# Optimization experiments

Measured on AMD Instinct MI355X. Metric: run time of the kernel, lower is better.

Reference implementation:

```python
import jax, jax.numpy as jnp
import numpy as np

N_Q = 8  # number of residual quantization levels


def setup_inputs() -> dict:
    key = jax.random.key(0)
    k1, k2 = jax.random.split(key)
    hidden_states = jax.random.normal(k1, (8192, 128), dtype=jnp.float32)
    codebooks = jax.random.normal(k2, (N_Q, 256, 128), dtype=jnp.float32)
    return {"hidden_states": hidden_states, "codebooks": codebooks}


def reference(hidden_states, codebooks):
    """Residual VQ encode: per level, nearest codebook entry by L2, subtract, accumulate.

    hidden_states: [N, D]; codebooks: [n_q, bins, D].
    Returns (codes [n_q, N] int, quantized [N, D]).
    """
    residual = hidden_states
    quantized = jnp.zeros_like(hidden_states)
    codes = []
    for i in range(N_Q):  # small fixed loop over structurally distinct levels
        codebook = codebooks[i]  # [bins, D]
        # squared L2 distance, same math as the original broadcasted form
        dist = jnp.sum((residual[:, None, :] - codebook[None, :, :]) ** 2, axis=-1)  # [N, bins]
        idx = jnp.argmin(dist, axis=-1)  # [N]
        chosen = codebook[idx]  # [N, D]
        quantized = quantized + chosen
        residual = residual - chosen
        codes.append(idx)
    return jnp.stack(codes, axis=0), quantized
```

## Files before the change

### kernel.cpp

```cpp
#include <hip/hip_runtime.h>

#define NQ 8
#define BINS 256
#define D 128
#define RPB 32
#define THREADS 1024
#define RSTRIDE 132
#define FREG 520

typedef short s8v __attribute__((ext_vector_type(8)));
typedef short s4v __attribute__((ext_vector_type(4)));
typedef float f4v __attribute__((ext_vector_type(4)));

static __device__ __forceinline__ unsigned short bf16_rtne(float x) {
    unsigned u = __float_as_uint(x);
    unsigned r = (u + 0x7fffu + ((u >> 16) & 1u)) >> 16;
    return (unsigned short)r;
}
static __device__ __forceinline__ float bf16_to_f(unsigned short h) {
    return __uint_as_float(((unsigned)h) << 16);
}
struct Split3 { short h, m, l; };
static __device__ __forceinline__ Split3 split3(float x) {
    Split3 s;
    unsigned short hb = bf16_rtne(x);
    float r1 = x - bf16_to_f(hb);
    unsigned short mb = bf16_rtne(r1);
    unsigned short lb = bf16_rtne(r1 - bf16_to_f(mb));
    s.h = (short)hb; s.m = (short)mb; s.l = (short)lb;
    return s;
}
static __device__ __forceinline__ unsigned long long u64min(unsigned long long a, unsigned long long b) {
    return a < b ? a : b;
}
static __device__ __forceinline__ unsigned dpp_row_min16(unsigned v) {
    unsigned t;
    t = (unsigned)__builtin_amdgcn_update_dpp(0, (int)v, 0xB1,  0xF, 0xF, true); v = v < t ? v : t;
    t = (unsigned)__builtin_amdgcn_update_dpp(0, (int)v, 0x4E,  0xF, 0xF, true); v = v < t ? v : t;
    t = (unsigned)__builtin_amdgcn_update_dpp(0, (int)v, 0x124, 0xF, 0xF, true); v = v < t ? v : t;
    t = (unsigned)__builtin_amdgcn_update_dpp(0, (int)v, 0x128, 0xF, 0xF, true); v = v < t ? v : t;
    return v;
}

__global__ __launch_bounds__(256) void rvq_prep(
    const float* __restrict__ cb, short* __restrict__ cb_hi,
    short* __restrict__ cb_mid, short* __restrict__ cb_lo,
    float* __restrict__ c2)
{
    __shared__ float st[16 * RSTRIDE];
    const int L = blockIdx.x >> 4;
    const int o = blockIdx.x & 15;
    const int t = threadIdx.x;

    const float4* src = (const float4*)(cb + ((size_t)L * BINS + o * 16) * D);
    #pragma unroll
    for (int i = 0; i < 2; ++i) {
        int f4 = i * 256 + t;
        int row = f4 >> 5, c4 = f4 & 31;
        float4 v = src[f4];
        float* d = &st[row * RSTRIDE + c4 * 4];
        d[0] = v.x; d[1] = v.y; d[2] = v.z; d[3] = v.w;
    }
    __syncthreads();

    const int bin = t >> 4;
    const int kc  = t & 15;
    const float* p = &st[bin * RSTRIDE + kc * 8];
    s8v h8, m8, l8;
    float s = 0.f;
    #pragma unroll
    for (int j = 0; j < 8; ++j) {
        float x = p[j];
        Split3 sp = split3(x);
        h8[j] = sp.h; m8[j] = sp.m; l8[j] = sp.l;
        s = fmaf(x, x, s);
    }
    int idx = (L * 16 + kc) * BINS + (o * 16 + bin);
    ((s8v*)cb_hi)[idx]  = h8;
    ((s8v*)cb_mid)[idx] = m8;
    ((s8v*)cb_lo)[idx]  = l8;
    s += __shfl_xor(s, 1, 64);
    s += __shfl_xor(s, 2, 64);
    s += __shfl_xor(s, 4, 64);
    s += __shfl_xor(s, 8, 64);
    if (kc == 0) c2[L * BINS + o * 16 + bin] = s;
}

static __device__ __forceinline__ void frag_store4(
    const float* rres, short* ah, short* am, short* al, int rr_, int g8, int half)
{
    s4v h4, m4, l4;
    #pragma unroll
    for (int j = 0; j < 4; ++j) {
        Split3 sp = split3(rres[j]);
        h4[j] = sp.h; m4[j] = sp.m; l4[j] = sp.l;
    }
    int q  = g8 & 3;
    int ks = g8 >> 2;
    int mt = rr_ >> 4;
    int r16 = rr_ & 15;
    int idx16 = q * 16 + ((r16 + 4 * q) & 15);
    int off = (mt * 4 + ks) * FREG + idx16 * 8 + half * 4;
    *(s4v*)&ah[off] = h4;
    *(s4v*)&am[off] = m4;
    *(s4v*)&al[off] = l4;
}

static __device__ __forceinline__ void issue_b(
    int lv, int bin, int quad,
    const s8v* __restrict__ bhp, const s8v* __restrict__ bmp, const s8v* __restrict__ blp,
    const float* __restrict__ c2p,
    s8v bh[4], s8v bm[4], s8v bl[4], float& c2v)
{
    c2v = c2p[lv * BINS + bin];
    #pragma unroll
    for (int ks = 0; ks < 4; ++ks) {
        int idx = (lv * 16 + ks * 4 + quad) * BINS + bin;
        bh[ks] = bhp[idx];
        bm[ks] = bmp[idx];
        bl[ks] = blp[idx];
    }
}

__global__ __launch_bounds__(THREADS, 4) void rvq_kernel(
    const float* __restrict__ hidden,
    const float* __restrict__ cb_f32,
    const short* __restrict__ cb_hi,
    const short* __restrict__ cb_mid,
    const short* __restrict__ cb_lo,
    const float* __restrict__ c2p,
    float* __restrict__ out_codes,
    float* __restrict__ out_quant,
    int N)
{
    __shared__ __align__(16) short ah[8 * FREG];
    __shared__ __align__(16) short am[8 * FREG];
    __shared__ __align__(16) short al[8 * FREG];
    __shared__ __align__(16) unsigned long long redw[RPB][18];

    const int t = threadIdx.x;
    const int w = t >> 6;
    const int l = t & 63;
    const int quad = l >> 4;
    const int m = l & 15;
    const int row0 = blockIdx.x * RPB;
    const int woff = w * 16;
    const int bin = woff + m;
    const int rr_  = t >> 5;
    const int gd   = t & 31;
    const int g8   = gd >> 1;
    const int half = gd & 1;
    const int dbase = g8 * 8 + half * 4;

    float rres[4], hreg[4];
    {
        const float4* hp = (const float4*)(hidden + (size_t)(row0 + rr_) * D + dbase);
        float4 v = *hp;
        hreg[0] = v.x; hreg[1] = v.y; hreg[2] = v.z; hreg[3] = v.w;
        rres[0] = v.x; rres[1] = v.y; rres[2] = v.z; rres[3] = v.w;
    }
    frag_store4(rres, ah, am, al, rr_, g8, half);

    const s8v* bhp = (const s8v*)cb_hi;
    const s8v* bmp = (const s8v*)cb_mid;
    const s8v* blp = (const s8v*)cb_lo;

    s8v bh[4], bm[4], bl[4];
    float c2v;
    issue_b(0, bin, quad, bhp, bmp, blp, c2p, bh, bm, bl, c2v);

    for (int level = 0; level < NQ; ++level) {
        __syncthreads();

        unsigned ucand[2][4];
        const int idx16 = quad * 16 + ((m + 4 * quad) & 15);
        #pragma unroll
        for (int mt = 0; mt < 2; ++mt) {
            f4v a0 = {0.f, 0.f, 0.f, 0.f};
            f4v a1 = {0.f, 0.f, 0.f, 0.f};
            f4v a2 = {0.f, 0.f, 0.f, 0.f};
            #pragma unroll
            for (int ks = 0; ks < 4; ++ks) {
                int off = (mt * 4 + ks) * FREG + idx16 * 8;
                s8v afh = *(const s8v*)&ah[off];
                s8v afm = *(const s8v*)&am[off];
                s8v afl = *(const s8v*)&al[off];
                a0 = __builtin_amdgcn_mfma_f32_16x16x32_bf16(afh, bh[ks], a0, 0, 0, 0);
                a1 = __builtin_amdgcn_mfma_f32_16x16x32_bf16(afh, bm[ks], a1, 0, 0, 0);
                a1 = __builtin_amdgcn_mfma_f32_16x16x32_bf16(afm, bh[ks], a1, 0, 0, 0);
                a2 = __builtin_amdgcn_mfma_f32_16x16x32_bf16(afm, bm[ks], a2, 0, 0, 0);
                a2 = __builtin_amdgcn_mfma_f32_16x16x32_bf16(afh, bl[ks], a2, 0, 0, 0);
                a2 = __builtin_amdgcn_mfma_f32_16x16x32_bf16(afl, bh[ks], a2, 0, 0, 0);
            }
            #pragma unroll
            for (int i = 0; i < 4; ++i) {
                float dot = a0[i] + (a1[i] + a2[i]);
                float k = fmaf(-2.f, dot, c2v);
                unsigned u = __float_as_uint(k);
                u = (u & 0x80000000u) ? ~u : (u | 0x80000000u);
                ucand[mt][i] = u;
            }
        }

        if (level + 1 < NQ)
            issue_b(level + 1, bin, quad, bhp, bmp, blp, c2p, bh, bm, bl, c2v);

        #pragma unroll
        for (int mt = 0; mt < 2; ++mt)
            #pragma unroll
            for (int i = 0; i < 4; ++i) {
                unsigned v = ucand[mt][i];
                unsigned r = dpp_row_min16(v);
                unsigned long long mk = __ballot(v == r);
                unsigned grp = (unsigned)(mk >> (quad * 16)) & 0xffffu;
                int bmin = woff + __builtin_ctz(grp);
                if (m == 0)
                    redw[mt * 16 + quad * 4 + i][w] =
                        ((unsigned long long)r << 32) | (unsigned)bmin;
            }
        __syncthreads();

        unsigned long long mn;
        {
            const ulonglong2* rp = (const ulonglong2*)&redw[rr_][0];
            ulonglong2 p0 = rp[0], p1 = rp[1], p2 = rp[2], p3 = rp[3];
            ulonglong2 p4 = rp[4], p5 = rp[5], p6 = rp[6], p7 = rp[7];
            unsigned long long a = u64min(u64min(u64min(p0.x, p0.y), u64min(p1.x, p1.y)),
                                          u64min(u64min(p2.x, p2.y), u64min(p3.x, p3.y)));
            unsigned long long b = u64min(u64min(u64min(p4.x, p4.y), u64min(p5.x, p5.y)),
                                          u64min(u64min(p6.x, p6.y), u64min(p7.x, p7.y)));
            mn = u64min(a, b);
        }
        const int wb = (int)(mn & 0xffffffffull);
        if (gd == 0)
            out_codes[(size_t)level * N + row0 + rr_] = (float)wb;

        {
            const float4* cp = (const float4*)(cb_f32 + ((size_t)level * BINS + wb) * D + dbase);
            float4 c = *cp;
            rres[0] -= c.x; rres[1] -= c.y; rres[2] -= c.z; rres[3] -= c.w;
        }
        if (level + 1 < NQ)
            frag_store4(rres, ah, am, al, rr_, g8, half);
    }

    {
        float4 q;
        q.x = hreg[0] - rres[0]; q.y = hreg[1] - rres[1];
        q.z = hreg[2] - rres[2]; q.w = hreg[3] - rres[3];
        *(float4*)(out_quant + (size_t)(row0 + rr_) * D + dbase) = q;
    }
}

extern "C" void kernel_launch(void* const* d_in, const int* in_sizes, int n_in,
                              void* d_out, int out_size, void* d_ws, size_t ws_size,
                              hipStream_t stream) {
    const float* hidden    = (const float*)d_in[0];
    const float* codebooks = (const float*)d_in[1];
    float* out = (float*)d_out;
    const int N = in_sizes[0] / D;
    float* out_codes = out;
    float* out_quant = out + (size_t)NQ * N;

    char* ws = (char*)d_ws;
    short* cb_hi  = (short*)ws;
    short* cb_mid = (short*)(ws +  512 * 1024);
    short* cb_lo  = (short*)(ws + 1024 * 1024);
    float* c2     = (float*)(ws + 1536 * 1024);

    rvq_prep<<<dim3(NQ * 16), 256, 0, stream>>>(codebooks, cb_hi, cb_mid, cb_lo, c2);
    rvq_kernel<<<dim3(N / RPB), THREADS, 0, stream>>>(
        hidden, codebooks, cb_hi, cb_mid, cb_lo, c2, out_codes, out_quant, N);
}
```

Baseline: 102.5 us.

## Remap waves so each owns 16 rows by 32 bins and simplify argmin reduction

Each wave now handles one 16-row M tile against 32 codebook bins, split into two N tiles. The wave keeps the residual fragments in registers and streams codebook fragments for the second N tile and the next level, instead of looping over both M tiles for 16 bins. MFMA operands are swapped so rows sit on lanes. The argmin becomes a per-lane packed u64 min plus two cross-lane shuffles, replacing four DPP min rounds and a ballot per candidate, and the shared-memory cross-wave reduction drops from 16 entries to 8. It also adds s_setprio around the MFMA block, and reloads the hidden input at the end instead of holding it in registers. The cost is more codebook loads issued per level, with less prefetch distance before they are needed.

New measurement: 201.8 us. 97.0% more time.

```diff
diff --git a/kernel.cpp b/kernel.cpp
--- a/kernel.cpp
+++ b/kernel.cpp
@@ -33,13 +33,12 @@
 static __device__ __forceinline__ unsigned long long u64min(unsigned long long a, unsigned long long b) {
     return a < b ? a : b;
 }
-static __device__ __forceinline__ unsigned dpp_row_min16(unsigned v) {
-    unsigned t;
-    t = (unsigned)__builtin_amdgcn_update_dpp(0, (int)v, 0xB1,  0xF, 0xF, true); v = v < t ? v : t;
-    t = (unsigned)__builtin_amdgcn_update_dpp(0, (int)v, 0x4E,  0xF, 0xF, true); v = v < t ? v : t;
-    t = (unsigned)__builtin_amdgcn_update_dpp(0, (int)v, 0x124, 0xF, 0xF, true); v = v < t ? v : t;
-    t = (unsigned)__builtin_amdgcn_update_dpp(0, (int)v, 0x128, 0xF, 0xF, true); v = v < t ? v : t;
-    return v;
+static __device__ __forceinline__ unsigned long long shfl_xor_u64(unsigned long long v, int mask) {
+    int lo = (int)(unsigned)(v & 0xffffffffull);
+    int hi = (int)(unsigned)(v >> 32);
+    lo = __shfl_xor(lo, mask, 64);
+    hi = __shfl_xor(hi, mask, 64);
+    return ((unsigned long long)(unsigned)hi << 32) | (unsigned)lo;
 }
 
 __global__ __launch_bounds__(256) void rvq_prep(
@@ -106,13 +105,13 @@
     *(s4v*)&al[off] = l4;
 }
 
-static __device__ __forceinline__ void issue_b(
-    int lv, int bin, int quad,
+static __device__ __forceinline__ void issue_cb(
+    int lv, int base16, int m, int quad,
     const s8v* __restrict__ bhp, const s8v* __restrict__ bmp, const s8v* __restrict__ blp,
     const float* __restrict__ c2p,
-    s8v bh[4], s8v bm[4], s8v bl[4], float& c2v)
-{
-    c2v = c2p[lv * BINS + bin];
+    s8v bh[4], s8v bm[4], s8v bl[4], float4& c2v)
+{
+    const int bin = base16 + m;
     #pragma unroll
     for (int ks = 0; ks < 4; ++ks) {
         int idx = (lv * 16 + ks * 4 + quad) * BINS + bin;
@@ -120,6 +119,7 @@
         bm[ks] = bmp[idx];
         bl[ks] = blp[idx];
     }
+    c2v = *(const float4*)(c2p + lv * BINS + base16 + quad * 4);
 }
 
 __global__ __launch_bounds__(THREADS, 4) void rvq_kernel(
@@ -136,27 +136,27 @@
     __shared__ __align__(16) short ah[8 * FREG];
     __shared__ __align__(16) short am[8 * FREG];
     __shared__ __align__(16) short al[8 * FREG];
-    __shared__ __align__(16) unsigned long long redw[RPB][18];
+    __shared__ __align__(16) unsigned long long redw[RPB][10];
 
     const int t = threadIdx.x;
     const int w = t >> 6;
     const int l = t & 63;
     const int quad = l >> 4;
     const int m = l & 15;
+    const int win  = w >> 1;
+    const int mt   = w & 1;
+    const int woff = win * 32;
     const int row0 = blockIdx.x * RPB;
-    const int woff = w * 16;
-    const int bin = woff + m;
     const int rr_  = t >> 5;
     const int gd   = t & 31;
     const int g8   = gd >> 1;
     const int half = gd & 1;
     const int dbase = g8 * 8 + half * 4;
 
-    float rres[4], hreg[4];
+    float rres[4];
     {
         const float4* hp = (const float4*)(hidden + (size_t)(row0 + rr_) * D + dbase);
         float4 v = *hp;
-        hreg[0] = v.x; hreg[1] = v.y; hreg[2] = v.z; hreg[3] = v.w;
         rres[0] = v.x; rres[1] = v.y; rres[2] = v.z; rres[3] = v.w;
     }
     frag_store4(rres, ah, am, al, rr_, g8, half);
@@ -166,70 +166,73 @@
     const s8v* blp = (const s8v*)cb_lo;
 
     s8v bh[4], bm[4], bl[4];
-    float c2v;
-    issue_b(0, bin, quad, bhp, bmp, blp, c2p, bh, bm, bl, c2v);
+    float4 c2v;
+    issue_cb(0, woff, m, quad, bhp, bmp, blp, c2p, bh, bm, bl, c2v);
 
     for (int level = 0; level < NQ; ++level) {
         __syncthreads();
 
-        unsigned ucand[2][4];
-        const int idx16 = quad * 16 + ((m + 4 * quad) & 15);
+        s8v rfh[4], rfm[4], rfl[4];
+        {
+            const int idx16 = quad * 16 + ((m + 4 * quad) & 15);
+            #pragma unroll
+            for (int ks = 0; ks < 4; ++ks) {
+                int off = (mt * 4 + ks) * FREG + idx16 * 8;
+                rfh[ks] = *(const s8v*)&ah[off];
+                rfm[ks] = *(const s8v*)&am[off];
+                rfl[ks] = *(const s8v*)&al[off];
+            }
+        }
+
+        unsigned long long best = ~0ull;
+
         #pragma unroll
-        for (int mt = 0; mt < 2; ++mt) {
+        for (int nt = 0; nt < 2; ++nt) {
             f4v a0 = {0.f, 0.f, 0.f, 0.f};
             f4v a1 = {0.f, 0.f, 0.f, 0.f};
             f4v a2 = {0.f, 0.f, 0.f, 0.f};
+            __builtin_amdgcn_s_setprio(1);
             #pragma unroll
             for (int ks = 0; ks < 4; ++ks) {
-                int off = (mt * 4 + ks) * FREG + idx16 * 8;
-                s8v afh = *(const s8v*)&ah[off];
-                s8v afm = *(const s8v*)&am[off];
-                s8v afl = *(const s8v*)&al[off];
-                a0 = __builtin_amdgcn_mfma_f32_16x16x32_bf16(afh, bh[ks], a0, 0, 0, 0);
-                a1 = __builtin_amdgcn_mfma_f32_16x16x32_bf16(afh, bm[ks], a1, 0, 0, 0);
-                a1 = __builtin_amdgcn_mfma_f32_16x16x32_bf16(afm, bh[ks], a1, 0, 0, 0);
-                a2 = __builtin_amdgcn_mfma_f32_16x16x32_bf16(afm, bm[ks], a2, 0, 0, 0);
-                a2 = __builtin_amdgcn_mfma_f32_16x16x32_bf16(afh, bl[ks], a2, 0, 0, 0);
-                a2 = __builtin_amdgcn_mfma_f32_16x16x32_bf16(afl, bh[ks], a2, 0, 0, 0);
+                a0 = __builtin_amdgcn_mfma_f32_16x16x32_bf16(bh[ks], rfh[ks], a0, 0, 0, 0);
+                a1 = __builtin_amdgcn_mfma_f32_16x16x32_bf16(bm[ks], rfh[ks], a1, 0, 0, 0);
+                a1 = __builtin_amdgcn_mfma_f32_16x16x32_bf16(bh[ks], rfm[ks], a1, 0, 0, 0);
+                a2 = __builtin_amdgcn_mfma_f32_16x16x32_bf16(bm[ks], rfm[ks], a2, 0, 0, 0);
+                a2 = __builtin_amdgcn_mfma_f32_16x16x32_bf16(bl[ks], rfh[ks], a2, 0, 0, 0);
+                a2 = __builtin_amdgcn_mfma_f32_16x16x32_bf16(bh[ks], rfl[ks], a2, 0, 0, 0);
             }
+            __builtin_amdgcn_s_setprio(0);
+            float4 c2cur = c2v;
+            const int binbase = woff + nt * 16 + quad * 4;
+
+            if (nt == 0)
+                issue_cb(level, woff + 16, m, quad, bhp, bmp, blp, c2p, bh, bm, bl, c2v);
+            else if (level + 1 < NQ)
+                issue_cb(level + 1, woff, m, quad, bhp, bmp, blp, c2p, bh, bm, bl, c2v);
+
+            const float* c2s = (const float*)&c2cur;
             #pragma unroll
             for (int i = 0; i < 4; ++i) {
                 float dot = a0[i] + (a1[i] + a2[i]);
-                float k = fmaf(-2.f, dot, c2v);
+                float k = fmaf(-2.f, dot, c2s[i]);
                 unsigned u = __float_as_uint(k);
                 u = (u & 0x80000000u) ? ~u : (u | 0x80000000u);
-                ucand[mt][i] = u;
+                best = u64min(best, ((unsigned long long)u << 32) | (unsigned)(binbase + i));
             }
         }
 
-        if (level + 1 < NQ)
-            issue_b(level + 1, bin, quad, bhp, bmp, blp, c2p, bh, bm, bl, c2v);
-
-        #pragma unroll
-        for (int mt = 0; mt < 2; ++mt)
-            #pragma unroll
-            for (int i = 0; i < 4; ++i) {
-                unsigned v = ucand[mt][i];
-                unsigned r = dpp_row_min16(v);
-                unsigned long long mk = __ballot(v == r);
-                unsigned grp = (unsigned)(mk >> (quad * 16)) & 0xffffu;
-                int bmin = woff + __builtin_ctz(grp);
-                if (m == 0)
-                    redw[mt * 16 + quad * 4 + i][w] =
-                        ((unsigned long long)r << 32) | (unsigned)bmin;
-            }
+        best = u64min(best, shfl_xor_u64(best, 16));
+        best = u64min(best, shfl_xor_u64(best, 32));
+        if (l < 16)
+            redw[mt * 16 + m][win] = best;
         __syncthreads();
 
         unsigned long long mn;
         {
             const ulonglong2* rp = (const ulonglong2*)&redw[rr_][0];
             ulonglong2 p0 = rp[0], p1 = rp[1], p2 = rp[2], p3 = rp[3];
-            ulonglong2 p4 = rp[4], p5 = rp[5], p6 = rp[6], p7 = rp[7];
-            unsigned long long a = u64min(u64min(u64min(p0.x, p0.y), u64min(p1.x, p1.y)),
-                                          u64min(u64min(p2.x, p2.y), u64min(p3.x, p3.y)));
-            unsigned long long b = u64min(u64min(u64min(p4.x, p4.y), u64min(p5.x, p5.y)),
-                                          u64min(u64min(p6.x, p6.y), u64min(p7.x, p7.y)));
-            mn = u64min(a, b);
+            mn = u64min(u64min(u64min(p0.x, p0.y), u64min(p1.x, p1.y)),
+                        u64min(u64min(p2.x, p2.y), u64min(p3.x, p3.y)));
         }
         const int wb = (int)(mn & 0xffffffffull);
         if (gd == 0)
@@ -245,9 +248,11 @@
     }
 
     {
+        const float4* hp = (const float4*)(hidden + (size_t)(row0 + rr_) * D + dbase);
+        float4 v = *hp;
         float4 q;
-        q.x = hreg[0] - rres[0]; q.y = hreg[1] - rres[1];
-        q.z = hreg[2] - rres[2]; q.w = hreg[3] - rres[3];
+        q.x = v.x - rres[0]; q.y = v.y - rres[1];
+        q.z = v.z - rres[2]; q.w = v.w - rres[3];
         *(float4*)(out_quant + (size_t)(row0 + rr_) * D + dbase) = q;
     }
 }
```
